# Kernel optimization log

Measured on AMD Instinct MI355X. Metric: run time of the kernel, lower is better.

## Reference

```python
import jax, jax.numpy as jnp
import numpy as np

EMBED = 768
HEADS = 12
HEAD_DIM = EMBED // HEADS
B, S = 2, 2048


def setup_inputs() -> dict:
    key = jax.random.key(0)
    ks = jax.random.split(key, 5)
    scale = 1.0 / np.sqrt(EMBED)
    return {
        "x": jax.random.normal(ks[0], (B, S, EMBED), dtype=jnp.float32),
        "w_q": jax.random.normal(ks[1], (EMBED, EMBED), dtype=jnp.float32) * scale,
        "b_q": jnp.zeros((EMBED,), dtype=jnp.float32),
        "w_k": jax.random.normal(ks[2], (EMBED, EMBED), dtype=jnp.float32) * scale,
        "b_k": jnp.zeros((EMBED,), dtype=jnp.float32),
        "w_v": jax.random.normal(ks[3], (EMBED, EMBED), dtype=jnp.float32) * scale,
        "b_v": jnp.zeros((EMBED,), dtype=jnp.float32),
        "w_o": jax.random.normal(ks[4], (EMBED, EMBED), dtype=jnp.float32) * scale,
        "b_o": jnp.zeros((EMBED,), dtype=jnp.float32),
    }


def reference(x, w_q, b_q, w_k, b_k, w_v, b_v, w_o, b_o):
    b, s, _ = x.shape
    # QKV projections (torch Linear: y = x @ W^T + b)
    q = x @ w_q.T + b_q
    k = x @ w_k.T + b_k
    v = x @ w_v.T + b_v
    # split heads -> [b, h, s, d]
    def split(t):
        return t.reshape(b, s, HEADS, HEAD_DIM).transpose(0, 2, 1, 3)
    q, k, v = split(q), split(k), split(v)
    scores = jnp.einsum("bhqd,bhkd->bhqk", q, k) / jnp.sqrt(
        jnp.asarray(HEAD_DIM, dtype=jnp.float32))
    probs = jax.nn.softmax(scores, axis=-1)
    out = jnp.einsum("bhqk,bhkd->bhqd", probs, v)
    out = out.transpose(0, 2, 1, 3).reshape(b, s, EMBED)
    return out @ w_o.T + b_o
```

## Files before the change

### kernel.cpp

```cpp
#include <hip/hip_runtime.h>
#include <math.h>

#define EMBED 768
#define HEADS 12
#define HDIM 64
#define BATCH 2
#define SEQ 2048
#define MTOT (BATCH*SEQ)

typedef short s8v __attribute__((ext_vector_type(8)));
typedef short s4v __attribute__((ext_vector_type(4)));
typedef float f4v __attribute__((ext_vector_type(4)));

__device__ __forceinline__ short f2bf(float f) {
    union { float f; unsigned u; } v; v.f = f;
    unsigned r = v.u + 0x7FFFu + ((v.u >> 16) & 1u);
    return (short)(r >> 16);
}

__device__ __forceinline__ unsigned pk2bf(float a, float b) {
    union { float f; unsigned u; } x, y; x.f = a; y.f = b;
    return ((y.u + 0x8000u) & 0xFFFF0000u) | ((x.u + 0x8000u) >> 16);
}

__device__ __forceinline__ void gll16(const short* g, short* l) {
    __builtin_amdgcn_global_load_lds((const __attribute__((address_space(1))) void*)g,
                                     (__attribute__((address_space(3))) void*)l, 16, 0, 0);
}

__global__ __launch_bounds__(256) void cvt_all(
        const float* __restrict__ x,  const float* __restrict__ wq,
        const float* __restrict__ wk, const float* __restrict__ wv,
        const float* __restrict__ wo,
        short* __restrict__ xb, short* __restrict__ wqb, short* __restrict__ wkb,
        short* __restrict__ wvb, short* __restrict__ wob) {
    const int seg = blockIdx.y;
    const float* src; short* dst; int n4;
    if      (seg == 0) { src = x;  dst = xb;  n4 = MTOT * EMBED / 4; }
    else if (seg == 1) { src = wq; dst = wqb; n4 = EMBED * EMBED / 4; }
    else if (seg == 2) { src = wk; dst = wkb; n4 = EMBED * EMBED / 4; }
    else if (seg == 3) { src = wv; dst = wvb; n4 = EMBED * EMBED / 4; }
    else               { src = wo; dst = wob; n4 = EMBED * EMBED / 4; }
    for (int i = blockIdx.x * 256 + threadIdx.x; i < n4; i += gridDim.x * 256) {
        float4 f = ((const float4*)src)[i];
        short4 o;
        o.x = f2bf(f.x); o.y = f2bf(f.y); o.z = f2bf(f.z); o.w = f2bf(f.w);
        ((short4*)dst)[i] = o;
    }
}

__global__ __launch_bounds__(256, 4) void gemm_qkv(const short* __restrict__ A,
        const short* __restrict__ Wq, const short* __restrict__ Wk, const short* __restrict__ Wv,
        const float* __restrict__ bq, const float* __restrict__ bk, const float* __restrict__ bv,
        short* __restrict__ Qo, short* __restrict__ Ko, short* __restrict__ Vo) {
    const int mode = blockIdx.z;
    const short* W    = (mode == 0) ? Wq : (mode == 1) ? Wk : Wv;
    const float* bias = (mode == 0) ? bq : (mode == 1) ? bk : bv;

    __shared__ short As[128 * 32];
    __shared__ short Ws[64 * 32];

    const int tid = threadIdx.x;
    const int lane = tid & 63, wid = tid >> 6;
    const int quad = lane >> 4, lr = lane & 15;
    const int m0 = blockIdx.x * 128, n0 = blockIdx.y * 64;
    const int wm = (wid >> 1) * 64, wn = (wid & 1) * 32;
    const int grow = lane >> 2, gcol = (lane & 3) * 8;

    f4v acc[4][2];
    for (int a = 0; a < 4; a++)
        for (int b = 0; b < 2; b++)
            for (int i = 0; i < 4; i++) acc[a][b][i] = 0.f;

    for (int k0 = 0; k0 < EMBED; k0 += 32) {
        gll16(&A[(m0 + wid * 16 + grow) * EMBED + k0 + gcol],       &As[wid * 512]);
        gll16(&A[(m0 + (wid + 4) * 16 + grow) * EMBED + k0 + gcol], &As[(wid + 4) * 512]);
        gll16(&W[(n0 + wid * 16 + grow) * EMBED + k0 + gcol],       &Ws[wid * 512]);
        __syncthreads();

        s8v af[4], bf[2];
        for (int mi = 0; mi < 4; mi++)
            af[mi] = *(const s8v*)&As[(wm + mi * 16 + lr) * 32 + quad * 8];
        for (int ni = 0; ni < 2; ni++)
            bf[ni] = *(const s8v*)&Ws[(wn + ni * 16 + lr) * 32 + quad * 8];
        for (int mi = 0; mi < 4; mi++)
            for (int ni = 0; ni < 2; ni++)
                acc[mi][ni] = __builtin_amdgcn_mfma_f32_16x16x32_bf16(af[mi], bf[ni], acc[mi][ni], 0, 0, 0);
        __syncthreads();
    }

    const int h = n0 >> 6;
    float bv2[2];
    for (int ni = 0; ni < 2; ni++) bv2[ni] = bias[n0 + wn + ni * 16 + lr];

    if (mode == 2) {
        for (int mi = 0; mi < 4; mi++) {
            int srow = m0 + wm + mi * 16 + quad * 4;
            int b = srow >> 11, s = srow & 2047;
            for (int ni = 0; ni < 2; ni++) {
                int d = wn + ni * 16 + lr;
                float v0 = acc[mi][ni][0] + bv2[ni], v1 = acc[mi][ni][1] + bv2[ni];
                float v2 = acc[mi][ni][2] + bv2[ni], v3 = acc[mi][ni][3] + bv2[ni];
                uint2 pk; pk.x = pk2bf(v0, v1); pk.y = pk2bf(v2, v3);
                *(uint2*)&Vo[(((long)(b * HEADS + h) * HDIM + d) * SEQ) + s] = pk;
            }
        }
    } else {
        short* Out = (mode == 0) ? Qo : Ko;
        for (int mi = 0; mi < 4; mi++) {
            for (int ni = 0; ni < 2; ni++) {
                for (int i = 0; i < 4; i++) {
                    int m = m0 + wm + mi * 16 + quad * 4 + i;
                    int b = m >> 11, s = m & 2047;
                    int d = wn + ni * 16 + lr;
                    Out[(((long)(b * HEADS + h) * SEQ + s) * HDIM) + d] =
                        f2bf(acc[mi][ni][i] + bv2[ni]);
                }
            }
        }
    }
}

__global__ __launch_bounds__(256, 4) void gemm_out(const short* __restrict__ A,
        const short* __restrict__ W, const float* __restrict__ bias,
        float* __restrict__ Out) {
    __shared__ short As[64 * 32];
    __shared__ short Ws[64 * 32];

    const int tid = threadIdx.x;
    const int lane = tid & 63, wid = tid >> 6;
    const int quad = lane >> 4, lr = lane & 15;
    const int m0 = blockIdx.x * 64, n0 = blockIdx.y * 64;
    const int wm = (wid >> 1) * 32, wn = (wid & 1) * 32;
    const int grow = lane >> 2, gcol = (lane & 3) * 8;

    f4v acc[2][2];
    for (int a = 0; a < 2; a++)
        for (int b = 0; b < 2; b++)
            for (int i = 0; i < 4; i++) acc[a][b][i] = 0.f;

    for (int k0 = 0; k0 < EMBED; k0 += 32) {
        gll16(&A[(m0 + wid * 16 + grow) * EMBED + k0 + gcol], &As[wid * 512]);
        gll16(&W[(n0 + wid * 16 + grow) * EMBED + k0 + gcol], &Ws[wid * 512]);
        __syncthreads();

        s8v af[2], bf[2];
        for (int mi = 0; mi < 2; mi++)
            af[mi] = *(const s8v*)&As[(wm + mi * 16 + lr) * 32 + quad * 8];
        for (int ni = 0; ni < 2; ni++)
            bf[ni] = *(const s8v*)&Ws[(wn + ni * 16 + lr) * 32 + quad * 8];
        for (int mi = 0; mi < 2; mi++)
            for (int ni = 0; ni < 2; ni++)
                acc[mi][ni] = __builtin_amdgcn_mfma_f32_16x16x32_bf16(af[mi], bf[ni], acc[mi][ni], 0, 0, 0);
        __syncthreads();
    }

    for (int mi = 0; mi < 2; mi++)
        for (int ni = 0; ni < 2; ni++)
            for (int i = 0; i < 4; i++) {
                int m = m0 + wm + mi * 16 + quad * 4 + i;
                int n = n0 + wn + ni * 16 + lr;
                Out[(long)m * EMBED + n] = acc[mi][ni][i] + bias[n];
            }
}

#define KSP 72
#define VSP 136
__global__ __launch_bounds__(256, 3) void flash_attn(const short* __restrict__ Q,
        const short* __restrict__ K, const short* __restrict__ Vt,
        short* __restrict__ Out) {
    extern __shared__ char pool[];
    short* Ks = (short*)pool;
    short* Vs = Ks + 128 * KSP;
    float* Om  = (float*)pool;
    float* lmB = (float*)pool + 64 * 68;
    float* lmT = lmB + 64;

    const int bh = blockIdx.y;
    const int tid = threadIdx.x, lane = tid & 63, wid = tid >> 6;
    const int quad = lane >> 4, lr = lane & 15;
    const int t = wid >> 1;
    const int qb = (wid & 1) * 32;
    const int q0 = blockIdx.x * 64;

    const short* Qb = Q  + (long)bh * SEQ * HDIM;
    const short* Kb = K  + (long)bh * SEQ * HDIM;
    const short* Vb = Vt + (long)bh * HDIM * SEQ;

    s8v qf[2][2];
    for (int mq = 0; mq < 2; mq++)
        for (int hh = 0; hh < 2; hh++)
            qf[mq][hh] = *(const s8v*)&Qb[(q0 + qb + mq * 16 + lr) * HDIM + hh * 32 + quad * 8];

    f4v o[2][4];
    for (int mq = 0; mq < 2; mq++)
        for (int dt = 0; dt < 4; dt++)
            for (int i = 0; i < 4; i++) o[mq][dt][i] = 0.f;
    float lsum[2] = {0.f, 0.f};

    const float SC = 0.125f;
    const float SB = -16.0f;

    union PU { unsigned u[4]; s8v s; };

    for (int r = 0; r < 16; r++) {
        const int k0 = r * 128;
        {
            int kr = tid >> 3, kc = (tid & 7) * 8;
            int vd = tid >> 4, kl = (tid & 15) * 8;
            int vt = kl >> 6, kk = kl & 63;
            int nt = kk >> 4, q4 = (kk >> 2) & 3;
            for (int p = 0; p < 4; p++) {
                int row = kr + p * 32;
                *(s8v*)&Ks[row * KSP + kc] = *(const s8v*)&Kb[(k0 + row) * HDIM + kc];
                int d = vd + p * 16;
                s8v v = *(const s8v*)&Vb[(long)d * SEQ + k0 + kl];
                int base = d * VSP + vt * 64 + nt * 4;
                *(s4v*)&Vs[base + q4 * 16]       = __builtin_shufflevector(v, v, 0, 1, 2, 3);
                *(s4v*)&Vs[base + (q4 + 1) * 16] = __builtin_shufflevector(v, v, 4, 5, 6, 7);
            }
        }
        __syncthreads();

        for (int np = 0; np < 2; np++) {
            s8v pfa[2], pfb[2];
            for (int half = 0; half < 2; half++) {
                const int nt = np * 2 + half;
                s8v kf0 = *(const s8v*)&Ks[(t * 64 + nt * 16 + lr) * KSP + quad * 8];
                s8v kf1 = *(const s8v*)&Ks[(t * 64 + nt * 16 + lr) * KSP + 32 + quad * 8];
                for (int mq = 0; mq < 2; mq++) {
                    f4v s = {0.f, 0.f, 0.f, 0.f};
                    s = __builtin_amdgcn_mfma_f32_16x16x32_bf16(kf0, qf[mq][0], s, 0, 0, 0);
                    s = __builtin_amdgcn_mfma_f32_16x16x32_bf16(kf1, qf[mq][1], s, 0, 0, 0);
                    float p0 = __expf(fmaf(s[0], SC, SB));
                    float p1 = __expf(fmaf(s[1], SC, SB));
                    float p2 = __expf(fmaf(s[2], SC, SB));
                    float p3 = __expf(fmaf(s[3], SC, SB));
                    lsum[mq] += (p0 + p1) + (p2 + p3);
                    PU pu;
                    if (half == 0) {
                        pu.u[0] = pk2bf(p0, p1); pu.u[1] = pk2bf(p2, p3);
                        pu.u[2] = 0u; pu.u[3] = 0u;
                        pfa[mq] = pu.s;
                    } else {
                        pu.u[0] = 0u; pu.u[1] = 0u;
                        pu.u[2] = pk2bf(p0, p1); pu.u[3] = pk2bf(p2, p3);
                        pfb[mq] = pu.s;
                    }
                }
            }
            for (int dt = 0; dt < 4; dt++) {
                s8v vf = *(const s8v*)&Vs[(dt * 16 + lr) * VSP + t * 64 + quad * 16 + np * 8];
                for (int mq = 0; mq < 2; mq++) {
                    o[mq][dt] = __builtin_amdgcn_mfma_f32_16x16x32_bf16(pfa[mq], vf, o[mq][dt], 0, 0, 0);
                    o[mq][dt] = __builtin_amdgcn_mfma_f32_16x16x32_bf16(pfb[mq], vf, o[mq][dt], 0, 0, 0);
                }
            }
        }
        __syncthreads();
    }

    for (int mq = 0; mq < 2; mq++) {
        lsum[mq] += __shfl_xor(lsum[mq], 16);
        lsum[mq] += __shfl_xor(lsum[mq], 32);
    }
    __syncthreads();
    if (wid >= 2) {
        for (int mq = 0; mq < 2; mq++) {
            for (int dt = 0; dt < 4; dt++)
                for (int i = 0; i < 4; i++)
                    Om[(qb + mq * 16 + quad * 4 + i) * 68 + dt * 16 + lr] = o[mq][dt][i];
            if (quad == 0) lmB[qb + mq * 16 + lr] = lsum[mq];
        }
    }
    __syncthreads();
    if (wid < 2) {
        for (int mq = 0; mq < 2; mq++) {
            float lt = lsum[mq] + lmB[qb + mq * 16 + lr];
            if (quad == 0) lmT[qb + mq * 16 + lr] = lt;
        }
    }
    __syncthreads();
    if (wid < 2) {
        const int b = bh / HEADS, h = bh % HEADS;
        for (int mq = 0; mq < 2; mq++) {
            float linv[4];
            for (int i = 0; i < 4; i++)
                linv[i] = 1.0f / lmT[qb + mq * 16 + quad * 4 + i];
            for (int dt = 0; dt < 4; dt++) {
                for (int i = 0; i < 4; i++) {
                    int ql = qb + mq * 16 + quad * 4 + i;
                    float val = (o[mq][dt][i] + Om[ql * 68 + dt * 16 + lr]) * linv[i];
                    int q = q0 + ql;
                    Out[((long)(b * SEQ + q)) * EMBED + h * HDIM + dt * 16 + lr] = f2bf(val);
                }
            }
        }
    }
}

extern "C" void kernel_launch(void* const* d_in, const int* in_sizes, int n_in,
                              void* d_out, int out_size, void* d_ws, size_t ws_size,
                              hipStream_t stream) {
    const float* x   = (const float*)d_in[0];
    const float* w_q = (const float*)d_in[1];
    const float* b_q = (const float*)d_in[2];
    const float* w_k = (const float*)d_in[3];
    const float* b_k = (const float*)d_in[4];
    const float* w_v = (const float*)d_in[5];
    const float* b_v = (const float*)d_in[6];
    const float* w_o = (const float*)d_in[7];
    const float* b_o = (const float*)d_in[8];

    short* x_bf   = (short*)d_ws;
    short* wq_bf  = x_bf  + MTOT * EMBED;
    short* wk_bf  = wq_bf + EMBED * EMBED;
    short* wv_bf  = wk_bf + EMBED * EMBED;
    short* wo_bf  = wv_bf + EMBED * EMBED;
    short* q_bf   = wo_bf + EMBED * EMBED;
    short* k_bf   = q_bf  + BATCH * HEADS * SEQ * HDIM;
    short* v_bf   = k_bf  + BATCH * HEADS * SEQ * HDIM;
    short* att_bf = v_bf  + BATCH * HEADS * SEQ * HDIM;

    cvt_all<<<dim3(1024, 5), 256, 0, stream>>>(x, w_q, w_k, w_v, w_o,
                                               x_bf, wq_bf, wk_bf, wv_bf, wo_bf);

    gemm_qkv<<<dim3(MTOT / 128, EMBED / 64, 3), 256, 0, stream>>>(
        x_bf, wq_bf, wk_bf, wv_bf, b_q, b_k, b_v, q_bf, k_bf, v_bf);

    flash_attn<<<dim3(SEQ / 64, BATCH * HEADS), 256,
                 (128 * KSP + 64 * VSP) * sizeof(short), stream>>>(q_bf, k_bf, v_bf, att_bf);

    gemm_out<<<dim3(MTOT / 64, EMBED / 64), 256, 0, stream>>>(
        att_bf, wo_bf, b_o, (float*)d_out);
}
```

Before: 184.1 us.

## Enlarge GEMM tiles, use async XOR-swizzled LDS loads and exp2 in attention

The QKV GEMM tile grows to 128x128 and the output GEMM tile to 128x64, so each block reuses more data and fewer blocks launch. The flash attention kernel now loads K and V into LDS with global_load_lds and an XOR swizzle instead of padded register copies. It packs P into one full-width MFMA operand instead of two half-zeroed ones, halving the PV MFMAs, and uses exp2 with prescaled constants. Occupancy is raised to 4 blocks per SM, and the larger tiles raise register pressure.

```diff
diff --git a/kernel.cpp b/kernel.cpp
--- a/kernel.cpp
+++ b/kernel.cpp
@@ -21,6 +21,14 @@
 __device__ __forceinline__ unsigned pk2bf(float a, float b) {
     union { float f; unsigned u; } x, y; x.f = a; y.f = b;
     return ((y.u + 0x8000u) & 0xFFFF0000u) | ((x.u + 0x8000u) >> 16);
+}
+
+__device__ __forceinline__ float fexp2(float x) {
+#if __has_builtin(__builtin_amdgcn_exp2f)
+    return __builtin_amdgcn_exp2f(x);
+#else
+    return exp2f(x);
+#endif
 }
 
 __device__ __forceinline__ void gll16(const short* g, short* l) {
@@ -58,6 +66,74 @@
     const float* bias = (mode == 0) ? bq : (mode == 1) ? bk : bv;
 
     __shared__ short As[128 * 32];
+    __shared__ short Ws[128 * 32];
+
+    const int tid = threadIdx.x;
+    const int lane = tid & 63, wid = tid >> 6;
+    const int quad = lane >> 4, lr = lane & 15;
+    const int m0 = blockIdx.x * 128, n0 = blockIdx.y * 128;
+    const int wm = (wid >> 1) * 64, wn = (wid & 1) * 64;
+    const int ar = lane >> 2, ac = (lane & 3) * 8;
+
+    f4v acc[4][4];
+    for (int a = 0; a < 4; a++)
+        for (int b = 0; b < 4; b++)
+            for (int i = 0; i < 4; i++) acc[a][b][i] = 0.f;
+
+    for (int k0 = 0; k0 < EMBED; k0 += 32) {
+        gll16(&A[(long)(m0 + wid * 32 + ar) * EMBED + k0 + ac],      &As[(wid * 32) * 32]);
+        gll16(&A[(long)(m0 + wid * 32 + 16 + ar) * EMBED + k0 + ac], &As[(wid * 32 + 16) * 32]);
+        gll16(&W[(long)(n0 + wid * 32 + ar) * EMBED + k0 + ac],      &Ws[(wid * 32) * 32]);
+        gll16(&W[(long)(n0 + wid * 32 + 16 + ar) * EMBED + k0 + ac], &Ws[(wid * 32 + 16) * 32]);
+        __syncthreads();
+
+        s8v af[4], bf[4];
+        for (int mi = 0; mi < 4; mi++)
+            af[mi] = *(const s8v*)&As[(wm + mi * 16 + lr) * 32 + quad * 8];
+        for (int ni = 0; ni < 4; ni++)
+            bf[ni] = *(const s8v*)&Ws[(wn + ni * 16 + lr) * 32 + quad * 8];
+        for (int mi = 0; mi < 4; mi++)
+            for (int ni = 0; ni < 4; ni++)
+                acc[mi][ni] = __builtin_amdgcn_mfma_f32_16x16x32_bf16(af[mi], bf[ni], acc[mi][ni], 0, 0, 0);
+        __syncthreads();
+    }
+
+    if (mode == 2) {
+        for (int mi = 0; mi < 4; mi++) {
+            int srow = m0 + wm + mi * 16 + quad * 4;
+            int b = srow >> 11, s = srow & 2047;
+            for (int ni = 0; ni < 4; ni++) {
+                int n = n0 + wn + ni * 16 + lr;
+                int h = n >> 6, d = n & 63;
+                float bb = bias[n];
+                uint2 pk;
+                pk.x = pk2bf(acc[mi][ni][0] + bb, acc[mi][ni][1] + bb);
+                pk.y = pk2bf(acc[mi][ni][2] + bb, acc[mi][ni][3] + bb);
+                *(uint2*)&Vo[(((long)(b * HEADS + h) * HDIM + d) * SEQ) + s] = pk;
+            }
+        }
+    } else {
+        short* Out = (mode == 0) ? Qo : Ko;
+        for (int mi = 0; mi < 4; mi++) {
+            for (int ni = 0; ni < 4; ni++) {
+                int n = n0 + wn + ni * 16 + lr;
+                int h = n >> 6, d = n & 63;
+                float bb = bias[n];
+                for (int i = 0; i < 4; i++) {
+                    int m = m0 + wm + mi * 16 + quad * 4 + i;
+                    int b = m >> 11, s = m & 2047;
+                    Out[(((long)(b * HEADS + h) * SEQ + s) * HDIM) + d] =
+                        f2bf(acc[mi][ni][i] + bb);
+                }
+            }
+        }
+    }
+}
+
+__global__ __launch_bounds__(256, 4) void gemm_out(const short* __restrict__ A,
+        const short* __restrict__ W, const float* __restrict__ bias,
+        float* __restrict__ Out) {
+    __shared__ short As[128 * 32];
     __shared__ short Ws[64 * 32];
 
     const int tid = threadIdx.x;
@@ -65,7 +141,7 @@
     const int quad = lane >> 4, lr = lane & 15;
     const int m0 = blockIdx.x * 128, n0 = blockIdx.y * 64;
     const int wm = (wid >> 1) * 64, wn = (wid & 1) * 32;
-    const int grow = lane >> 2, gcol = (lane & 3) * 8;
+    const int ar = lane >> 2, ac = (lane & 3) * 8;
 
     f4v acc[4][2];
     for (int a = 0; a < 4; a++)
@@ -73,9 +149,9 @@
             for (int i = 0; i < 4; i++) acc[a][b][i] = 0.f;
 
     for (int k0 = 0; k0 < EMBED; k0 += 32) {
-        gll16(&A[(m0 + wid * 16 + grow) * EMBED + k0 + gcol],       &As[wid * 512]);
-        gll16(&A[(m0 + (wid + 4) * 16 + grow) * EMBED + k0 + gcol], &As[(wid + 4) * 512]);
-        gll16(&W[(n0 + wid * 16 + grow) * EMBED + k0 + gcol],       &Ws[wid * 512]);
+        gll16(&A[(long)(m0 + wid * 32 + ar) * EMBED + k0 + ac],      &As[(wid * 32) * 32]);
+        gll16(&A[(long)(m0 + wid * 32 + 16 + ar) * EMBED + k0 + ac], &As[(wid * 32 + 16) * 32]);
+        gll16(&W[(long)(n0 + wid * 16 + ar) * EMBED + k0 + ac],      &Ws[(wid * 16) * 32]);
         __syncthreads();
 
         s8v af[4], bf[2];
@@ -89,73 +165,7 @@
         __syncthreads();
     }
 
-    const int h = n0 >> 6;
-    float bv2[2];
-    for (int ni = 0; ni < 2; ni++) bv2[ni] = bias[n0 + wn + ni * 16 + lr];
-
-    if (mode == 2) {
-        for (int mi = 0; mi < 4; mi++) {
-            int srow = m0 + wm + mi * 16 + quad * 4;
-            int b = srow >> 11, s = srow & 2047;
-            for (int ni = 0; ni < 2; ni++) {
-                int d = wn + ni * 16 + lr;
-                float v0 = acc[mi][ni][0] + bv2[ni], v1 = acc[mi][ni][1] + bv2[ni];
-                float v2 = acc[mi][ni][2] + bv2[ni], v3 = acc[mi][ni][3] + bv2[ni];
-                uint2 pk; pk.x = pk2bf(v0, v1); pk.y = pk2bf(v2, v3);
-                *(uint2*)&Vo[(((long)(b * HEADS + h) * HDIM + d) * SEQ) + s] = pk;
-            }
-        }
-    } else {
-        short* Out = (mode == 0) ? Qo : Ko;
-        for (int mi = 0; mi < 4; mi++) {
-            for (int ni = 0; ni < 2; ni++) {
-                for (int i = 0; i < 4; i++) {
-                    int m = m0 + wm + mi * 16 + quad * 4 + i;
-                    int b = m >> 11, s = m & 2047;
-                    int d = wn + ni * 16 + lr;
-                    Out[(((long)(b * HEADS + h) * SEQ + s) * HDIM) + d] =
-                        f2bf(acc[mi][ni][i] + bv2[ni]);
-                }
-            }
-        }
-    }
-}
-
-__global__ __launch_bounds__(256, 4) void gemm_out(const short* __restrict__ A,
-        const short* __restrict__ W, const float* __restrict__ bias,
-        float* __restrict__ Out) {
-    __shared__ short As[64 * 32];
-    __shared__ short Ws[64 * 32];
-
-    const int tid = threadIdx.x;
-    const int lane = tid & 63, wid = tid >> 6;
-    const int quad = lane >> 4, lr = lane & 15;
-    const int m0 = blockIdx.x * 64, n0 = blockIdx.y * 64;
-    const int wm = (wid >> 1) * 32, wn = (wid & 1) * 32;
-    const int grow = lane >> 2, gcol = (lane & 3) * 8;
-
-    f4v acc[2][2];
-    for (int a = 0; a < 2; a++)
-        for (int b = 0; b < 2; b++)
-            for (int i = 0; i < 4; i++) acc[a][b][i] = 0.f;
-
-    for (int k0 = 0; k0 < EMBED; k0 += 32) {
-        gll16(&A[(m0 + wid * 16 + grow) * EMBED + k0 + gcol], &As[wid * 512]);
-        gll16(&W[(n0 + wid * 16 + grow) * EMBED + k0 + gcol], &Ws[wid * 512]);
-        __syncthreads();
-
-        s8v af[2], bf[2];
-        for (int mi = 0; mi < 2; mi++)
-            af[mi] = *(const s8v*)&As[(wm + mi * 16 + lr) * 32 + quad * 8];
-        for (int ni = 0; ni < 2; ni++)
-            bf[ni] = *(const s8v*)&Ws[(wn + ni * 16 + lr) * 32 + quad * 8];
-        for (int mi = 0; mi < 2; mi++)
-            for (int ni = 0; ni < 2; ni++)
-                acc[mi][ni] = __builtin_amdgcn_mfma_f32_16x16x32_bf16(af[mi], bf[ni], acc[mi][ni], 0, 0, 0);
-        __syncthreads();
-    }
-
-    for (int mi = 0; mi < 2; mi++)
+    for (int mi = 0; mi < 4; mi++)
         for (int ni = 0; ni < 2; ni++)
             for (int i = 0; i < 4; i++) {
                 int m = m0 + wm + mi * 16 + quad * 4 + i;
@@ -164,14 +174,12 @@
             }
 }
 
-#define KSP 72
-#define VSP 136
-__global__ __launch_bounds__(256, 3) void flash_attn(const short* __restrict__ Q,
+__global__ __launch_bounds__(256, 4) void flash_attn(const short* __restrict__ Q,
         const short* __restrict__ K, const short* __restrict__ Vt,
         short* __restrict__ Out) {
     extern __shared__ char pool[];
     short* Ks = (short*)pool;
-    short* Vs = Ks + 128 * KSP;
+    short* Vs = Ks + 128 * 64;
     float* Om  = (float*)pool;
     float* lmB = (float*)pool + 64 * 68;
     float* lmT = lmB + 64;
@@ -198,63 +206,57 @@
             for (int i = 0; i < 4; i++) o[mq][dt][i] = 0.f;
     float lsum[2] = {0.f, 0.f};
 
-    const float SC = 0.125f;
-    const float SB = -16.0f;
-
-    union PU { unsigned u[4]; s8v s; };
+    const float SC2 = 0.125f * 1.44269504f;
+    const float SB2 = -16.0f * 1.44269504f;
+
+    const int krow = lane >> 3;
+    const int kslot = (lane & 7) ^ (krow & 7);
+    const int vrow = lane >> 4;
 
     for (int r = 0; r < 16; r++) {
         const int k0 = r * 128;
-        {
-            int kr = tid >> 3, kc = (tid & 7) * 8;
-            int vd = tid >> 4, kl = (tid & 15) * 8;
-            int vt = kl >> 6, kk = kl & 63;
-            int nt = kk >> 4, q4 = (kk >> 2) & 3;
-            for (int p = 0; p < 4; p++) {
-                int row = kr + p * 32;
-                *(s8v*)&Ks[row * KSP + kc] = *(const s8v*)&Kb[(k0 + row) * HDIM + kc];
-                int d = vd + p * 16;
-                s8v v = *(const s8v*)&Vb[(long)d * SEQ + k0 + kl];
-                int base = d * VSP + vt * 64 + nt * 4;
-                *(s4v*)&Vs[base + q4 * 16]       = __builtin_shufflevector(v, v, 0, 1, 2, 3);
-                *(s4v*)&Vs[base + (q4 + 1) * 16] = __builtin_shufflevector(v, v, 4, 5, 6, 7);
-            }
+        for (int i = 0; i < 4; i++) {
+            int r0 = wid * 32 + i * 8;
+            gll16(&Kb[(long)(k0 + r0 + krow) * HDIM + kslot * 8], &Ks[r0 * HDIM]);
+            int d0 = wid * 16 + i * 4;
+            int vslot = (lane & 15) ^ ((i * 4 + vrow) & 15);
+            gll16(&Vb[(long)(d0 + vrow) * SEQ + k0 + vslot * 8], &Vs[d0 * 128]);
         }
         __syncthreads();
 
         for (int np = 0; np < 2; np++) {
-            s8v pfa[2], pfb[2];
+            unsigned pw[2][4];
             for (int half = 0; half < 2; half++) {
                 const int nt = np * 2 + half;
-                s8v kf0 = *(const s8v*)&Ks[(t * 64 + nt * 16 + lr) * KSP + quad * 8];
-                s8v kf1 = *(const s8v*)&Ks[(t * 64 + nt * 16 + lr) * KSP + 32 + quad * 8];
+                const int row = t * 64 + nt * 16 + lr;
+                s8v kf0 = *(const s8v*)&Ks[row * 64 + ((quad ^ (lr & 7)) * 8)];
+                s8v kf1 = *(const s8v*)&Ks[row * 64 + (((4 + quad) ^ (lr & 7)) * 8)];
                 for (int mq = 0; mq < 2; mq++) {
                     f4v s = {0.f, 0.f, 0.f, 0.f};
                     s = __builtin_amdgcn_mfma_f32_16x16x32_bf16(kf0, qf[mq][0], s, 0, 0, 0);
                     s = __builtin_amdgcn_mfma_f32_16x16x32_bf16(kf1, qf[mq][1], s, 0, 0, 0);
-                    float p0 = __expf(fmaf(s[0], SC, SB));
-                    float p1 = __expf(fmaf(s[1], SC, SB));
-                    float p2 = __expf(fmaf(s[2], SC, SB));
-                    float p3 = __expf(fmaf(s[3], SC, SB));
+                    float p0 = fexp2(fmaf(s[0], SC2, SB2));
+                    float p1 = fexp2(fmaf(s[1], SC2, SB2));
+                    float p2 = fexp2(fmaf(s[2], SC2, SB2));
+                    float p3 = fexp2(fmaf(s[3], SC2, SB2));
                     lsum[mq] += (p0 + p1) + (p2 + p3);
-                    PU pu;
-                    if (half == 0) {
-                        pu.u[0] = pk2bf(p0, p1); pu.u[1] = pk2bf(p2, p3);
-                        pu.u[2] = 0u; pu.u[3] = 0u;
-                        pfa[mq] = pu.s;
-                    } else {
-                        pu.u[0] = 0u; pu.u[1] = 0u;
-                        pu.u[2] = pk2bf(p0, p1); pu.u[3] = pk2bf(p2, p3);
-                        pfb[mq] = pu.s;
-                    }
+                    pw[mq][half * 2]     = pk2bf(p0, p1);
+                    pw[mq][half * 2 + 1] = pk2bf(p2, p3);
                 }
             }
+            s8v pf[2];
+            pf[0] = *(s8v*)&pw[0][0];
+            pf[1] = *(s8v*)&pw[1][0];
             for (int dt = 0; dt < 4; dt++) {
-                s8v vf = *(const s8v*)&Vs[(dt * 16 + lr) * VSP + t * 64 + quad * 16 + np * 8];
-                for (int mq = 0; mq < 2; mq++) {
-                    o[mq][dt] = __builtin_amdgcn_mfma_f32_16x16x32_bf16(pfa[mq], vf, o[mq][dt], 0, 0, 0);
-                    o[mq][dt] = __builtin_amdgcn_mfma_f32_16x16x32_bf16(pfb[mq], vf, o[mq][dt], 0, 0, 0);
-                }
+                const int d = dt * 16 + lr;
+                int cbase = t * 8 + np * 4 + (quad >> 1);
+                int c0 = cbase ^ lr;
+                int c1 = (cbase + 2) ^ lr;
+                s4v v0 = *(const s4v*)&Vs[d * 128 + c0 * 8 + (quad & 1) * 4];
+                s4v v1 = *(const s4v*)&Vs[d * 128 + c1 * 8 + (quad & 1) * 4];
+                s8v vf = __builtin_shufflevector(v0, v1, 0, 1, 2, 3, 4, 5, 6, 7);
+                o[0][dt] = __builtin_amdgcn_mfma_f32_16x16x32_bf16(pf[0], vf, o[0][dt], 0, 0, 0);
+                o[1][dt] = __builtin_amdgcn_mfma_f32_16x16x32_bf16(pf[1], vf, o[1][dt], 0, 0, 0);
             }
         }
         __syncthreads();
@@ -325,12 +327,12 @@
     cvt_all<<<dim3(1024, 5), 256, 0, stream>>>(x, w_q, w_k, w_v, w_o,
                                                x_bf, wq_bf, wk_bf, wv_bf, wo_bf);
 
-    gemm_qkv<<<dim3(MTOT / 128, EMBED / 64, 3), 256, 0, stream>>>(
+    gemm_qkv<<<dim3(MTOT / 128, EMBED / 128, 3), 256, 0, stream>>>(
         x_bf, wq_bf, wk_bf, wv_bf, b_q, b_k, b_v, q_bf, k_bf, v_bf);
 
-    flash_attn<<<dim3(SEQ / 64, BATCH * HEADS), 256,
-                 (128 * KSP + 64 * VSP) * sizeof(short), stream>>>(q_bf, k_bf, v_bf, att_bf);
-
-    gemm_out<<<dim3(MTOT / 64, EMBED / 64), 256, 0, stream>>>(
+    flash_attn<<<dim3(SEQ / 64, BATCH * HEADS), 256, 32768, stream>>>(
+        q_bf, k_bf, v_bf, att_bf);
+
+    gemm_out<<<dim3(MTOT / 128, EMBED / 64), 256, 0, stream>>>(
         att_bf, wo_bf, b_o, (float*)d_out);
 }
```

After: 164.1 us. 1.12x faster.
